# Kernel optimization log

Hardware: AMD Instinct MI355X
Metric: run time of the kernel (lower is better)

Reference implementation:

```python
import jax, jax.numpy as jnp
import numpy as np

# config constants (from init_kwargs config['masking'])
MASK_RATIO = 0.15
SPAN_MIN = 5
SPAN_MAX = 20


def _generate_batch_masks(key, batch_size, seq_len):
    """Span-based random masking, exact-count adjusted. [B, S] bool."""
    target_masked = int(seq_len * MASK_RATIO)              # static
    avg_span = (SPAN_MIN + SPAN_MAX) / 2.0
    n_spans = max(1, int(target_masked / avg_span * 2))    # estimated_spans
    k_len, k_start, k_noise = jax.random.split(key, 3)

    span_lengths = jax.random.randint(k_len, (batch_size, n_spans), SPAN_MIN, SPAN_MAX + 1)
    starts = jax.random.randint(k_start, (batch_size, n_spans), 0, max(1, seq_len - SPAN_MIN))
    ends = jnp.minimum(starts + span_lengths, seq_len)

    # Span coverage via +1/-1 scatter + cumsum (equivalent to the per-span
    # boolean scatter loop in the torch code, fully on-device).
    b_idx = jnp.arange(batch_size)[:, None]
    delta = jnp.zeros((batch_size, seq_len + 1), jnp.int32)
    delta = delta.at[b_idx, starts].add(1).at[b_idx, ends].add(-1)
    coverage = jnp.cumsum(delta[:, :seq_len], axis=1) > 0   # [B, S] bool

    # Exact-count adjustment: equivalent to randomly removing excess masked
    # positions / randomly adding unmasked positions until count == target.
    # Masked positions get score in (1,2), unmasked in (0,1); top-k = keep a
    # random masked subset, fill remainder with random unmasked positions.
    noise = jax.random.uniform(k_noise, (batch_size, seq_len))
    score = coverage.astype(jnp.float32) + noise
    _, top_idx = jax.lax.top_k(score, target_masked)        # [B, target]
    masks = jnp.zeros((batch_size, seq_len), bool).at[b_idx, top_idx].set(True)
    return masks


def setup_inputs() -> dict:
    key = jax.random.key(0)
    k1, k2 = jax.random.split(key)
    features = jax.random.normal(k1, (128, 16384, 6), dtype=jnp.float32)
    mask_token = jax.random.normal(k2, (6,), dtype=jnp.float32) * 0.02
    return {"features": features, "mask_token": mask_token}


def reference(features, mask_token):
    B, S, F = features.shape
    key = jax.random.key(1234)  # plays the role of the module's torch.Generator seed
    masks = _generate_batch_masks(key, B, S)
    # _apply_valid_mask_vectorized: only mask non-NaN positions (channel 0)
    valid = ~jnp.isnan(features[:, :, 0])
    masks = masks & valid
    # apply_mask_to_features: replace masked positions with mask_token
    masked_features = jnp.where(masks[:, :, None], mask_token[None, None, :], features)
    return masked_features
```

## Files before the change

kernel.cpp:

```cpp
#include <hip/hip_runtime.h>
#include <stdint.h>

constexpr int NB = 128;
constexpr int SEQ = 16384;
constexpr int NF = 6;
constexpr int NSPANS = 393;
constexpr uint32_t TGT = 2457u;
constexpr int ROWF = SEQ * NF;
constexpr int ROWF4 = ROWF / 4;
constexpr int TOT4 = NB * ROWF4;
constexpr int COPY_BLOCKS = TOT4 / 3072;

constexpr int FM_OFF = 0;
constexpr int FM_DW = NB * (SEQ / 32);
constexpr size_t WS_BYTES = (size_t)FM_DW * 4;

struct Keys {
  uint32_t klo0, klo1;
  uint32_t khi_s0, khi_s1;
  uint32_t klo_s0, klo_s1;
  uint32_t kn0, kn1;
};

__host__ __device__ inline void tf2x32(uint32_t k0, uint32_t k1,
                                       uint32_t x0, uint32_t x1,
                                       uint32_t& o0, uint32_t& o1) {
  uint32_t ks[3] = {k0, k1, k0 ^ k1 ^ 0x1BD11BDAu};
  uint32_t a = x0 + ks[0], b = x1 + ks[1];
  const uint32_t rot[2][4] = {{13u,15u,26u,6u},{17u,29u,16u,24u}};
#pragma unroll
  for (int i = 0; i < 5; ++i) {
    const uint32_t* r = rot[i & 1];
#pragma unroll
    for (int j = 0; j < 4; ++j) {
      a += b;
      b = (b << r[j]) | (b >> (32u - r[j]));
      b ^= a;
    }
    a += ks[(i + 1) % 3];
    b += ks[(i + 2) % 3] + (uint32_t)(i + 1);
  }
  o0 = a; o1 = b;
}

__device__ inline uint32_t rbits(uint32_t k0, uint32_t k1, uint32_t j) {
  uint32_t o0, o1;
  tf2x32(k0, k1, 0u, j, o0, o1);
  return o0 ^ o1;
}

__global__ __launch_bounds__(1024)
void fused_kernel(const float* __restrict__ feat, float* __restrict__ out,
                  uint32_t* __restrict__ ws, Keys K) {
  __shared__ uint32_t hist[4096];
  __shared__ uint32_t cov[SEQ / 32];
  __shared__ uint32_t fm[SEQ / 32];
  __shared__ uint32_t wsum[16], ssum[16];
  __shared__ int tielist[256];
  __shared__ uint32_t sH, sA, sT, sN;
  __shared__ int tieCnt;

  const int t = threadIdx.x;

  if (blockIdx.x >= (unsigned)NB) {
    const uint32_t n = blockIdx.x - NB;
    const float4* f4 = (const float4*)feat + (size_t)n * 3072;
    float4* o4 = (float4*)out + (size_t)n * 3072;
    o4[t] = f4[t];
    o4[t + 1024] = f4[t + 1024];
    o4[t + 2048] = f4[t + 2048];
    return;
  }

  const int lane = t & 63;
  const int wid = t >> 6;
  const uint32_t b = blockIdx.x;

  for (int i = t; i < 4096; i += 1024) hist[i] = 0u;
  if (t < SEQ / 32) cov[t] = 0u;
  if (t == 0) tieCnt = 0;
  __syncthreads();

  if (t < NSPANS) {
    uint32_t j = b * (uint32_t)NSPANS + (uint32_t)t;
    uint32_t lenb = rbits(K.klo0, K.klo1, j);
    uint32_t len = 5u + (lenb & 15u);
    uint32_t hb = rbits(K.khi_s0, K.khi_s1, j);
    uint32_t lb = rbits(K.klo_s0, K.klo_s1, j);
    const uint32_t span = 16379u;
    uint32_t start = ((hb % span) * 400u + (lb % span)) % span;
    uint32_t end = start + len; if (end > (uint32_t)SEQ) end = SEQ;
    uint32_t w0 = start >> 5, w1 = (end - 1u) >> 5;
    for (uint32_t w = w0; w <= w1; ++w) {
      uint32_t bs = (w == w0) ? (start & 31u) : 0u;
      uint32_t be = (w == w1) ? ((end - 1u) & 31u) : 31u;
      uint32_t n = be - bs + 1u;
      uint32_t m = (n >= 32u) ? 0xFFFFFFFFu : (((1u << n) - 1u) << bs);
      atomicOr(&cov[w], m);
    }
  }
  __syncthreads();

  const uint32_t jb = b << 14;
  uint32_t sr[16];
#pragma unroll
  for (int i = 0; i < 16; ++i) {
    int s = (i << 10) + t;
    uint32_t bits = rbits(K.kn0, K.kn1, jb + (uint32_t)s);
    uint32_t si = (bits >> 9) + (((cov[s >> 5] >> (s & 31)) & 1u) << 23);
    sr[i] = si;
    atomicAdd(&hist[si >> 12], 1u);
  }
  __syncthreads();

  {
    uint32_t mysum = 0;
#pragma unroll
    for (int i = 0; i < 4; ++i) mysum += hist[t * 4 + i];
    uint32_t v = mysum;
#pragma unroll
    for (int off = 1; off < 64; off <<= 1) {
      uint32_t n = __shfl_down(v, off, 64);
      if (lane + off < 64) v += n;
    }
    if (lane == 0) wsum[wid] = v;
    __syncthreads();
    if (t < 16) {
      uint32_t w = wsum[t];
#pragma unroll
      for (int off = 1; off < 16; off <<= 1) {
        uint32_t n = __shfl_down(w, off, 64);
        if (t + off < 16) w += n;
      }
      ssum[t] = w;
    }
    __syncthreads();
    uint32_t mine = v + (ssum[wid] - wsum[wid]);
    uint32_t above = mine - mysum;
    if (above < TGT && TGT <= mine) {
      uint32_t run = above;
      for (int hb = t * 4 + 3; hb >= t * 4; --hb) {
        uint32_t c = hist[hb];
        if (run + c >= TGT) { sH = (uint32_t)hb; sA = run; break; }
        run += c;
      }
    }
  }
  __syncthreads();
  uint32_t H = sH;
  uint32_t targetB = TGT - sA;

  for (int i = t; i < 4096; i += 1024) hist[i] = 0u;
  __syncthreads();

#pragma unroll
  for (int i = 0; i < 16; ++i) {
    uint32_t si = sr[i];
    if ((si >> 12) == H) atomicAdd(&hist[si & 4095u], 1u);
  }
  __syncthreads();
  {
    uint32_t mysum = 0;
#pragma unroll
    for (int i = 0; i < 4; ++i) mysum += hist[t * 4 + i];
    uint32_t v = mysum;
#pragma unroll
    for (int off = 1; off < 64; off <<= 1) {
      uint32_t n = __shfl_down(v, off, 64);
      if (lane + off < 64) v += n;
    }
    if (lane == 0) wsum[wid] = v;
    __syncthreads();
    if (t < 16) {
      uint32_t w = wsum[t];
#pragma unroll
      for (int off = 1; off < 16; off <<= 1) {
        uint32_t n = __shfl_down(w, off, 64);
        if (t + off < 16) w += n;
      }
      ssum[t] = w;
    }
    __syncthreads();
    uint32_t mine = v + (ssum[wid] - wsum[wid]);
    uint32_t above = mine - mysum;
    if (above < targetB && targetB <= mine) {
      uint32_t run = above;
      for (int lb = t * 4 + 3; lb >= t * 4; --lb) {
        uint32_t c = hist[lb];
        if (run + c >= targetB) {
          sT = (H << 12) | (uint32_t)lb;
          sN = targetB - run;
          break;
        }
        run += c;
      }
    }
  }
  __syncthreads();
  uint32_t T = sT, need = sN;

#pragma unroll
  for (int i = 0; i < 16; ++i) {
    int s = (i << 10) + t;
    uint32_t si = sr[i];
    unsigned long long bal = __ballot(si > T);
    if (si == T) {
      int idx = atomicAdd(&tieCnt, 1);
      if (idx < 256) tielist[idx] = s;
    }
    if (lane == 0)       fm[s >> 5] = (uint32_t)bal;
    else if (lane == 32) fm[s >> 5] = (uint32_t)(bal >> 32);
  }
  __syncthreads();
  int tc = tieCnt < 256 ? tieCnt : 256;
  if (t < tc) {
    int s = tielist[t];
    uint32_t rank = 0;
    for (int j = 0; j < tc; ++j) rank += (tielist[j] < s) ? 1u : 0u;
    if (rank < need) atomicOr(&fm[s >> 5], 1u << (s & 31));
  }
  __syncthreads();
  if (t < SEQ / 32) ws[FM_OFF + (b << 9) + t] = fm[t];
}

__global__ __launch_bounds__(256)
void fixup_kernel(const float* __restrict__ feat, const float* __restrict__ tok,
                  const uint32_t* __restrict__ ws, float* __restrict__ out) {
  int g = blockIdx.x * 256 + threadIdx.x;
  uint32_t w = ws[FM_OFF + g];
  if (!w) return;
  float t0 = tok[0], t1 = tok[1], t2 = tok[2], t3 = tok[3], t4 = tok[4], t5 = tok[5];
  size_t basePos = (size_t)g * 32;
  while (w) {
    int bit = __ffs(w) - 1;
    w &= w - 1u;
    size_t p = basePos + (size_t)bit;
    float c0 = feat[p * 6];
    if (!(c0 != c0)) {
      float* o = out + p * 6;
      o[0] = t0; o[1] = t1; o[2] = t2; o[3] = t3; o[4] = t4; o[5] = t5;
    }
  }
}


__device__ inline uint32_t score_int(const Keys& K, uint32_t b, int s,
                                     const uint32_t* cov) {
  uint32_t j = b * (uint32_t)SEQ + (uint32_t)s;
  uint32_t bits = rbits(K.kn0, K.kn1, j);
  return (bits >> 9) + (((cov[s >> 5] >> (s & 31)) & 1u) << 23);
}

__global__ __launch_bounds__(256)
void mask_kernel(const float* __restrict__ feat, const float* __restrict__ tok,
                 float* __restrict__ out, Keys K) {
  __shared__ uint32_t cov[SEQ / 32];
  __shared__ uint32_t fm[SEQ / 32];
  __shared__ uint32_t hist[4096];
  __shared__ uint32_t part[256];
  __shared__ uint32_t sH, sA, sT, sN;

  const int t = threadIdx.x;
  const uint32_t b = blockIdx.x;

  for (int i = t; i < 4096; i += 256) hist[i] = 0u;
  for (int i = t; i < SEQ / 32; i += 256) cov[i] = 0u;
  __syncthreads();

  for (int i = t; i < NSPANS; i += 256) {
    uint32_t j = b * (uint32_t)NSPANS + (uint32_t)i;
    uint32_t lenb = rbits(K.klo0, K.klo1, j);
    uint32_t len = 5u + (lenb & 15u);
    uint32_t hb = rbits(K.khi_s0, K.khi_s1, j);
    uint32_t lb = rbits(K.klo_s0, K.klo_s1, j);
    const uint32_t span = 16379u;
    uint32_t start = ((hb % span) * 400u + (lb % span)) % span;
    uint32_t end = start + len; if (end > (uint32_t)SEQ) end = SEQ;
    uint32_t w0 = start >> 5, w1 = (end - 1u) >> 5;
    for (uint32_t w = w0; w <= w1; ++w) {
      uint32_t bs = (w == w0) ? (start & 31u) : 0u;
      uint32_t be = (w == w1) ? ((end - 1u) & 31u) : 31u;
      uint32_t n = be - bs + 1u;
      uint32_t m = (n >= 32u) ? 0xFFFFFFFFu : (((1u << n) - 1u) << bs);
      atomicOr(&cov[w], m);
    }
  }
  __syncthreads();

  for (int q = 0; q < 64; ++q) {
    uint32_t si = score_int(K, b, t + (q << 8), cov);
    atomicAdd(&hist[si >> 12], 1u);
  }
  __syncthreads();
  {
    uint32_t sum = 0;
#pragma unroll
    for (int i = 0; i < 16; ++i) sum += hist[t * 16 + i];
    part[t] = sum;
    __syncthreads();
    for (int off = 1; off < 256; off <<= 1) {
      uint32_t v = (t + off < 256) ? part[t + off] : 0u;
      __syncthreads();
      part[t] += v;
      __syncthreads();
    }
    uint32_t above = (t < 255) ? part[t + 1] : 0u;
    uint32_t mine = part[t];
    if (above < TGT && TGT <= mine) {
      uint32_t run = above;
      for (int hb = t * 16 + 15; hb >= t * 16; --hb) {
        uint32_t c = hist[hb];
        if (run + c >= TGT) { sH = (uint32_t)hb; sA = run; break; }
        run += c;
      }
    }
  }
  __syncthreads();
  uint32_t H = sH;
  uint32_t targetB = TGT - sA;

  for (int i = t; i < 4096; i += 256) hist[i] = 0u;
  __syncthreads();
  for (int q = 0; q < 64; ++q) {
    uint32_t si = score_int(K, b, t + (q << 8), cov);
    if ((si >> 12) == H) atomicAdd(&hist[si & 4095u], 1u);
  }
  __syncthreads();
  {
    uint32_t sum = 0;
#pragma unroll
    for (int i = 0; i < 16; ++i) sum += hist[t * 16 + i];
    part[t] = sum;
    __syncthreads();
    for (int off = 1; off < 256; off <<= 1) {
      uint32_t v = (t + off < 256) ? part[t + off] : 0u;
      __syncthreads();
      part[t] += v;
      __syncthreads();
    }
    uint32_t above = (t < 255) ? part[t + 1] : 0u;
    uint32_t mine = part[t];
    if (above < targetB && targetB <= mine) {
      uint32_t run = above;
      for (int lb = t * 16 + 15; lb >= t * 16; --lb) {
        uint32_t c = hist[lb];
        if (run + c >= targetB) { sT = (H << 12) | (uint32_t)lb; sN = targetB - run; break; }
        run += c;
      }
    }
  }
  __syncthreads();
  uint32_t T = sT, need = sN;

  const float* rowf = feat + (size_t)b * ROWF;
  {
    int base = t << 6;
    uint32_t cnt = 0;
    for (int i = 0; i < 64; ++i) cnt += (score_int(K, b, base + i, cov) == T) ? 1u : 0u;
    part[t] = cnt;
    __syncthreads();
    for (int off = 1; off < 256; off <<= 1) {
      uint32_t v = (t >= off) ? part[t - off] : 0u;
      __syncthreads();
      part[t] += v;
      __syncthreads();
    }
    uint32_t r = part[t] - cnt;
    uint32_t w0 = 0, w1 = 0;
    for (int i = 0; i < 64; ++i) {
      int s = base + i;
      uint32_t si = score_int(K, b, s, cov);
      bool tie = (si == T);
      bool a = (si > T) || (tie && r < need);
      r += tie ? 1u : 0u;
      float f0 = rowf[s * 6];
      a = a && !(f0 != f0);
      if (i < 32) w0 |= ((uint32_t)a) << i;
      else        w1 |= ((uint32_t)a) << (i - 32);
    }
    fm[2 * t] = w0;
    fm[2 * t + 1] = w1;
  }
  __syncthreads();

  float tk[NF];
#pragma unroll
  for (int c = 0; c < NF; ++c) tk[c] = tok[c];
  float* rowo = out + (size_t)b * ROWF;
  const float4* rf4 = (const float4*)rowf;
  float4* ro4 = (float4*)rowo;
  for (int q = t; q < ROWF4; q += 256) {
    float4 v = rf4[q];
    float vv[4] = {v.x, v.y, v.z, v.w};
    int e = q * 4;
#pragma unroll
    for (int k = 0; k < 4; ++k) {
      int ee = e + k;
      int p = ee / 6;
      int c = ee - p * 6;
      if ((fm[p >> 5] >> (p & 31)) & 1u) vv[k] = tk[c];
    }
    ro4[q] = make_float4(vv[0], vv[1], vv[2], vv[3]);
  }
}

extern "C" void kernel_launch(void* const* d_in, const int* in_sizes, int n_in,
                              void* d_out, int out_size, void* d_ws, size_t ws_size,
                              hipStream_t stream) {
  const float* feat = (const float*)d_in[0];
  const float* tok = (const float*)d_in[1];
  float* out = (float*)d_out;

  uint32_t klen0, klen1, kst0, kst1, kn0, kn1;
  tf2x32(0u, 1234u, 0u, 0u, klen0, klen1);
  tf2x32(0u, 1234u, 0u, 1u, kst0, kst1);
  tf2x32(0u, 1234u, 0u, 2u, kn0, kn1);
  uint32_t lh0, lh1, ll0, ll1;
  tf2x32(klen0, klen1, 0u, 0u, lh0, lh1);
  tf2x32(klen0, klen1, 0u, 1u, ll0, ll1);
  (void)lh0; (void)lh1;
  uint32_t sh0, sh1, sl0, sl1;
  tf2x32(kst0, kst1, 0u, 0u, sh0, sh1);
  tf2x32(kst0, kst1, 0u, 1u, sl0, sl1);
  Keys K{ ll0, ll1, sh0, sh1, sl0, sl1, kn0, kn1 };

  if (ws_size >= WS_BYTES) {
    uint32_t* ws = (uint32_t*)d_ws;
    hipLaunchKernelGGL(fused_kernel, dim3(NB + COPY_BLOCKS), dim3(1024), 0, stream,
                       feat, out, ws, K);
    hipLaunchKernelGGL(fixup_kernel, dim3(FM_DW / 256), dim3(256), 0, stream,
                       feat, tok, ws, out);
  } else {
    hipLaunchKernelGGL(mask_kernel, dim3(NB), dim3(256), 0, stream, feat, tok, out, K);
  }
}
```

Measured before the change: 112.1 us.

## Fuse mask apply into per-row-half blocks, dropping separate copy and fixup kernels

Replaces the concurrent copy blocks plus a fixup kernel with a single kernel where two blocks per row each recompute the row's mask and then write their half of the row, substituting the mask token inline with vectorized nontemporal stores. This removes the second launch, the workspace bitmask round-trip and the scattered fixup writes. In exchange the mask selection is computed twice per row, and the bulk copy now waits behind mask generation instead of overlapping with it. The fallback path without a workspace is also removed.

```diff
diff --git a/kernel.cpp b/kernel.cpp
--- a/kernel.cpp
+++ b/kernel.cpp
@@ -3,17 +3,13 @@
 
 constexpr int NB = 128;
 constexpr int SEQ = 16384;
-constexpr int NF = 6;
 constexpr int NSPANS = 393;
 constexpr uint32_t TGT = 2457u;
-constexpr int ROWF = SEQ * NF;
+constexpr int ROWF = SEQ * 6;
 constexpr int ROWF4 = ROWF / 4;
-constexpr int TOT4 = NB * ROWF4;
-constexpr int COPY_BLOCKS = TOT4 / 3072;
-
-constexpr int FM_OFF = 0;
-constexpr int FM_DW = NB * (SEQ / 32);
-constexpr size_t WS_BYTES = (size_t)FM_DW * 4;
+constexpr int HALF4 = ROWF4 / 2;
+
+typedef float f32x4 __attribute__((ext_vector_type(4)));
 
 struct Keys {
   uint32_t klo0, klo1;
@@ -50,8 +46,8 @@
 }
 
 __global__ __launch_bounds__(1024)
-void fused_kernel(const float* __restrict__ feat, float* __restrict__ out,
-                  uint32_t* __restrict__ ws, Keys K) {
+void rowpair_kernel(const float* __restrict__ feat, const float* __restrict__ tok,
+                    float* __restrict__ out, Keys K) {
   __shared__ uint32_t hist[4096];
   __shared__ uint32_t cov[SEQ / 32];
   __shared__ uint32_t fm[SEQ / 32];
@@ -61,20 +57,11 @@
   __shared__ int tieCnt;
 
   const int t = threadIdx.x;
-
-  if (blockIdx.x >= (unsigned)NB) {
-    const uint32_t n = blockIdx.x - NB;
-    const float4* f4 = (const float4*)feat + (size_t)n * 3072;
-    float4* o4 = (float4*)out + (size_t)n * 3072;
-    o4[t] = f4[t];
-    o4[t + 1024] = f4[t + 1024];
-    o4[t + 2048] = f4[t + 2048];
-    return;
-  }
-
   const int lane = t & 63;
   const int wid = t >> 6;
-  const uint32_t b = blockIdx.x;
+  const uint32_t bid = blockIdx.x;
+  const uint32_t b = bid >> 1;
+  const int h = (int)(bid & 1u);
 
   for (int i = t; i < 4096; i += 1024) hist[i] = 0u;
   if (t < SEQ / 32) cov[t] = 0u;
@@ -220,187 +207,64 @@
     if (rank < need) atomicOr(&fm[s >> 5], 1u << (s & 31));
   }
   __syncthreads();
-  if (t < SEQ / 32) ws[FM_OFF + (b << 9) + t] = fm[t];
-}
-
-__global__ __launch_bounds__(256)
-void fixup_kernel(const float* __restrict__ feat, const float* __restrict__ tok,
-                  const uint32_t* __restrict__ ws, float* __restrict__ out) {
-  int g = blockIdx.x * 256 + threadIdx.x;
-  uint32_t w = ws[FM_OFF + g];
-  if (!w) return;
-  float t0 = tok[0], t1 = tok[1], t2 = tok[2], t3 = tok[3], t4 = tok[4], t5 = tok[5];
-  size_t basePos = (size_t)g * 32;
-  while (w) {
-    int bit = __ffs(w) - 1;
-    w &= w - 1u;
-    size_t p = basePos + (size_t)bit;
-    float c0 = feat[p * 6];
-    if (!(c0 != c0)) {
-      float* o = out + p * 6;
-      o[0] = t0; o[1] = t1; o[2] = t2; o[3] = t3; o[4] = t4; o[5] = t5;
-    }
-  }
-}
-
-
-__device__ inline uint32_t score_int(const Keys& K, uint32_t b, int s,
-                                     const uint32_t* cov) {
-  uint32_t j = b * (uint32_t)SEQ + (uint32_t)s;
-  uint32_t bits = rbits(K.kn0, K.kn1, j);
-  return (bits >> 9) + (((cov[s >> 5] >> (s & 31)) & 1u) << 23);
-}
-
-__global__ __launch_bounds__(256)
-void mask_kernel(const float* __restrict__ feat, const float* __restrict__ tok,
-                 float* __restrict__ out, Keys K) {
-  __shared__ uint32_t cov[SEQ / 32];
-  __shared__ uint32_t fm[SEQ / 32];
-  __shared__ uint32_t hist[4096];
-  __shared__ uint32_t part[256];
-  __shared__ uint32_t sH, sA, sT, sN;
-
-  const int t = threadIdx.x;
-  const uint32_t b = blockIdx.x;
-
-  for (int i = t; i < 4096; i += 256) hist[i] = 0u;
-  for (int i = t; i < SEQ / 32; i += 256) cov[i] = 0u;
-  __syncthreads();
-
-  for (int i = t; i < NSPANS; i += 256) {
-    uint32_t j = b * (uint32_t)NSPANS + (uint32_t)i;
-    uint32_t lenb = rbits(K.klo0, K.klo1, j);
-    uint32_t len = 5u + (lenb & 15u);
-    uint32_t hb = rbits(K.khi_s0, K.khi_s1, j);
-    uint32_t lb = rbits(K.klo_s0, K.klo_s1, j);
-    const uint32_t span = 16379u;
-    uint32_t start = ((hb % span) * 400u + (lb % span)) % span;
-    uint32_t end = start + len; if (end > (uint32_t)SEQ) end = SEQ;
-    uint32_t w0 = start >> 5, w1 = (end - 1u) >> 5;
-    for (uint32_t w = w0; w <= w1; ++w) {
-      uint32_t bs = (w == w0) ? (start & 31u) : 0u;
-      uint32_t be = (w == w1) ? ((end - 1u) & 31u) : 31u;
-      uint32_t n = be - bs + 1u;
-      uint32_t m = (n >= 32u) ? 0xFFFFFFFFu : (((1u << n) - 1u) << bs);
-      atomicOr(&cov[w], m);
-    }
-  }
-  __syncthreads();
-
-  for (int q = 0; q < 64; ++q) {
-    uint32_t si = score_int(K, b, t + (q << 8), cov);
-    atomicAdd(&hist[si >> 12], 1u);
-  }
-  __syncthreads();
+
   {
-    uint32_t sum = 0;
-#pragma unroll
-    for (int i = 0; i < 16; ++i) sum += hist[t * 16 + i];
-    part[t] = sum;
-    __syncthreads();
-    for (int off = 1; off < 256; off <<= 1) {
-      uint32_t v = (t + off < 256) ? part[t + off] : 0u;
-      __syncthreads();
-      part[t] += v;
-      __syncthreads();
-    }
-    uint32_t above = (t < 255) ? part[t + 1] : 0u;
-    uint32_t mine = part[t];
-    if (above < TGT && TGT <= mine) {
-      uint32_t run = above;
-      for (int hb = t * 16 + 15; hb >= t * 16; --hb) {
-        uint32_t c = hist[hb];
-        if (run + c >= TGT) { sH = (uint32_t)hb; sA = run; break; }
-        run += c;
-      }
-    }
-  }
-  __syncthreads();
-  uint32_t H = sH;
-  uint32_t targetB = TGT - sA;
-
-  for (int i = t; i < 4096; i += 256) hist[i] = 0u;
-  __syncthreads();
-  for (int q = 0; q < 64; ++q) {
-    uint32_t si = score_int(K, b, t + (q << 8), cov);
-    if ((si >> 12) == H) atomicAdd(&hist[si & 4095u], 1u);
-  }
-  __syncthreads();
-  {
-    uint32_t sum = 0;
-#pragma unroll
-    for (int i = 0; i < 16; ++i) sum += hist[t * 16 + i];
-    part[t] = sum;
-    __syncthreads();
-    for (int off = 1; off < 256; off <<= 1) {
-      uint32_t v = (t + off < 256) ? part[t + off] : 0u;
-      __syncthreads();
-      part[t] += v;
-      __syncthreads();
-    }
-    uint32_t above = (t < 255) ? part[t + 1] : 0u;
-    uint32_t mine = part[t];
-    if (above < targetB && targetB <= mine) {
-      uint32_t run = above;
-      for (int lb = t * 16 + 15; lb >= t * 16; --lb) {
-        uint32_t c = hist[lb];
-        if (run + c >= targetB) { sT = (H << 12) | (uint32_t)lb; sN = targetB - run; break; }
-        run += c;
-      }
-    }
-  }
-  __syncthreads();
-  uint32_t T = sT, need = sN;
-
-  const float* rowf = feat + (size_t)b * ROWF;
-  {
-    int base = t << 6;
-    uint32_t cnt = 0;
-    for (int i = 0; i < 64; ++i) cnt += (score_int(K, b, base + i, cov) == T) ? 1u : 0u;
-    part[t] = cnt;
-    __syncthreads();
-    for (int off = 1; off < 256; off <<= 1) {
-      uint32_t v = (t >= off) ? part[t - off] : 0u;
-      __syncthreads();
-      part[t] += v;
-      __syncthreads();
-    }
-    uint32_t r = part[t] - cnt;
-    uint32_t w0 = 0, w1 = 0;
-    for (int i = 0; i < 64; ++i) {
-      int s = base + i;
-      uint32_t si = score_int(K, b, s, cov);
-      bool tie = (si == T);
-      bool a = (si > T) || (tie && r < need);
-      r += tie ? 1u : 0u;
-      float f0 = rowf[s * 6];
-      a = a && !(f0 != f0);
-      if (i < 32) w0 |= ((uint32_t)a) << i;
-      else        w1 |= ((uint32_t)a) << (i - 32);
-    }
-    fm[2 * t] = w0;
-    fm[2 * t + 1] = w1;
-  }
-  __syncthreads();
-
-  float tk[NF];
-#pragma unroll
-  for (int c = 0; c < NF; ++c) tk[c] = tok[c];
-  float* rowo = out + (size_t)b * ROWF;
-  const float4* rf4 = (const float4*)rowf;
-  float4* ro4 = (float4*)rowo;
-  for (int q = t; q < ROWF4; q += 256) {
-    float4 v = rf4[q];
-    float vv[4] = {v.x, v.y, v.z, v.w};
-    int e = q * 4;
-#pragma unroll
-    for (int k = 0; k < 4; ++k) {
-      int ee = e + k;
-      int p = ee / 6;
-      int c = ee - p * 6;
-      if ((fm[p >> 5] >> (p & 31)) & 1u) vv[k] = tk[c];
-    }
-    ro4[q] = make_float4(vv[0], vv[1], vv[2], vv[3]);
+    const float t0 = tok[0], t1 = tok[1], t2 = tok[2];
+    const float t3 = tok[3], t4 = tok[4], t5 = tok[5];
+    const size_t rowBase4 = (size_t)b * ROWF4 + (size_t)h * HALF4;
+    const float* rowf = feat + (size_t)b * ROWF;
+    const f32x4* rf4 = (const f32x4*)feat + rowBase4;
+    f32x4* ro4 = (f32x4*)out + rowBase4;
+    const int qbase = h * HALF4;
+
+#pragma unroll
+    for (int batch = 0; batch < 3; ++batch) {
+      f32x4 v0, v1, v2, v3;
+      const int q0 = t + (batch * 4) * 1024;
+      v0 = rf4[q0];
+      v1 = rf4[q0 + 1024];
+      v2 = rf4[q0 + 2048];
+      v3 = rf4[q0 + 3072];
+
+      f32x4 vv[4] = {v0, v1, v2, v3};
+#pragma unroll
+      for (int j = 0; j < 4; ++j) {
+        const int qrow = qbase + q0 + j * 1024;
+        const int e = qrow * 4;
+        const int p0 = e / 6;
+        const int c0 = e - p0 * 6;
+        const int p1 = (p0 + 1 < SEQ) ? p0 + 1 : SEQ - 1;
+        const uint32_t w0 = fm[p0 >> 5];
+        const uint32_t w1 = fm[p1 >> 5];
+        bool m0 = (w0 >> (p0 & 31)) & 1u;
+        bool m1 = (w1 >> (p1 & 31)) & 1u;
+        if (m0) {
+          float c0v = rowf[p0 * 6];
+          m0 = !(c0v != c0v);
+        }
+        if (m1) {
+          float c1v = rowf[p1 * 6];
+          m1 = !(c1v != c1v);
+        }
+        const bool is0 = (c0 == 0), is2 = (c0 == 2);
+        const float a0 = is0 ? t0 : (is2 ? t2 : t4);
+        const float a1 = is0 ? t1 : (is2 ? t3 : t5);
+        const float a2 = is0 ? t2 : (is2 ? t4 : t0);
+        const float a3 = is0 ? t3 : (is2 ? t5 : t1);
+        const bool u01 = m0;
+        const bool u23 = (!is0 && !is2) ? m1 : m0;
+        f32x4 v = vv[j];
+        v.x = u01 ? a0 : v.x;
+        v.y = u01 ? a1 : v.y;
+        v.z = u23 ? a2 : v.z;
+        v.w = u23 ? a3 : v.w;
+        vv[j] = v;
+      }
+      __builtin_nontemporal_store(vv[0], &ro4[q0]);
+      __builtin_nontemporal_store(vv[1], &ro4[q0 + 1024]);
+      __builtin_nontemporal_store(vv[2], &ro4[q0 + 2048]);
+      __builtin_nontemporal_store(vv[3], &ro4[q0 + 3072]);
+    }
   }
 }
 
@@ -424,13 +288,6 @@
   tf2x32(kst0, kst1, 0u, 1u, sl0, sl1);
   Keys K{ ll0, ll1, sh0, sh1, sl0, sl1, kn0, kn1 };
 
-  if (ws_size >= WS_BYTES) {
-    uint32_t* ws = (uint32_t*)d_ws;
-    hipLaunchKernelGGL(fused_kernel, dim3(NB + COPY_BLOCKS), dim3(1024), 0, stream,
-                       feat, out, ws, K);
-    hipLaunchKernelGGL(fixup_kernel, dim3(FM_DW / 256), dim3(256), 0, stream,
-                       feat, tok, ws, out);
-  } else {
-    hipLaunchKernelGGL(mask_kernel, dim3(NB), dim3(256), 0, stream, feat, tok, out, K);
-  }
-}
+  hipLaunchKernelGGL(rowpair_kernel, dim3(2 * NB), dim3(1024), 0, stream,
+                     feat, tok, out, K);
+}
```

New measurement: 115.1 us. 1.03x slower.
